# Kernel tuning notes

Measured on AMD Instinct MI355X. Metric: run time of the kernel, lower is better.

Reference implementation:

```python
import jax, jax.numpy as jnp
import numpy as np

NUM_LEVELS = 16
LEVEL_DIM = 2
BASE_RES = 32
PER_LEVEL_SCALE = 2.0
TABLE_SIZE = 2 ** 19  # padded size of every level's table
RES = np.array([int(BASE_RES * PER_LEVEL_SCALE ** i) for i in range(NUM_LEVELS)], dtype=np.float32)
SIZES = np.minimum(RES.astype(np.float64) ** 3, TABLE_SIZE).astype(np.float32)  # true table sizes
NEAR, FAR, NUM_SAMPLES = 0.1, 1.5, 64
N_RAYS = 16384


def _xavier(key, fin, fout):
    lim = float(np.sqrt(6.0 / (fin + fout)))
    return jax.random.uniform(key, (fin, fout), jnp.float32, -lim, lim)


def setup_inputs() -> dict:
    key = jax.random.key(0)
    ks = jax.random.split(key, 12)
    rays_o = jax.random.uniform(ks[0], (N_RAYS, 3), jnp.float32, -0.5, 0.5)
    d = jax.random.normal(ks[1], (N_RAYS, 3), jnp.float32)
    rays_d = d / jnp.linalg.norm(d, axis=-1, keepdims=True)
    tables = jax.random.uniform(ks[2], (NUM_LEVELS, TABLE_SIZE, LEVEL_DIM), jnp.float32, -1e-4, 1e-4)
    return {
        'rays_o': rays_o, 'rays_d': rays_d, 'tables': tables,
        'Wg0': _xavier(ks[3], 32, 64), 'bg0': jnp.zeros((64,), jnp.float32),
        'Wg1': _xavier(ks[4], 64, 64), 'bg1': jnp.zeros((64,), jnp.float32),
        'Wd': _xavier(ks[5], 64, 16), 'bd': jnp.zeros((16,), jnp.float32),
        'Wc0': _xavier(ks[6], 24, 64), 'bc0': jnp.zeros((64,), jnp.float32),
        'Wc1': _xavier(ks[7], 64, 64), 'bc1': jnp.zeros((64,), jnp.float32),
        'Wc2': _xavier(ks[8], 64, 64), 'bc2': jnp.zeros((64,), jnp.float32),
        'Wch': _xavier(ks[9], 64, 3), 'bch': jnp.zeros((3,), jnp.float32),
    }


def _hash_encode(pts, tables):
    # pts: [N, S, 3] in roughly [-1, 1]; tables: [L, T, 2]
    res = jnp.asarray(RES)            # [L]
    sizes = jnp.asarray(SIZES)        # [L]
    scaled = (pts[..., None, :] + 1.0) / 2.0 * (res[:, None] - 1.0)     # [N,S,L,3]
    scaled = jnp.clip(scaled, 0.0, res[:, None] - 1.0)
    # torch computes the flat index in float then .long() (truncation), then clamps to table size
    idx_f = scaled[..., 0] * res * res + scaled[..., 1] * res + scaled[..., 2]  # [N,S,L]
    idx = jnp.minimum(idx_f, sizes - 1.0).astype(jnp.int32)
    feats = tables[jnp.arange(NUM_LEVELS)[None, None, :], idx]          # [N,S,L,2]
    return feats.reshape(feats.shape[:-2] + (NUM_LEVELS * LEVEL_DIM,))  # [N,S,32]


def _sh_encode(d):
    # degree-4 encoder in the source only ever builds 9 features
    x, y, z = d[..., 0], d[..., 1], d[..., 2]
    return jnp.stack([jnp.full_like(x, 0.5), x, y, z,
                      x * y, x * z, y * z, x * x - y * y, 3.0 * z * z - 1.0], axis=-1)  # [N,9]


def reference(rays_o, rays_d, tables, Wg0, bg0, Wg1, bg1, Wd, bd,
              Wc0, bc0, Wc1, bc1, Wc2, bc2, Wch, bch):
    n = rays_o.shape[0]
    # --- stratified-free (eval mode) sampling along rays ---
    t = jnp.linspace(0.0, 1.0, NUM_SAMPLES, dtype=jnp.float32)
    z_vals = jnp.broadcast_to(NEAR + (FAR - NEAR) * t, (n, NUM_SAMPLES))           # [N,S]
    pts = rays_o[:, None, :] + rays_d[:, None, :] * z_vals[..., None]              # [N,S,3]
    # --- LoDAwareNeRF forward ---
    feats = _hash_encode(pts, tables)                                              # [N,S,32]
    h = jax.nn.relu(feats @ Wg0 + bg0)
    h = jax.nn.relu(h @ Wg1 + bg1)
    geo = h @ Wd + bd                                                              # [N,S,16]
    density = jax.nn.softplus(geo[..., 0] - 1.0)                                   # [N,S]
    geo_feat = geo[..., 1:]                                                        # [N,S,15]
    dir_f = jnp.broadcast_to(_sh_encode(rays_d)[:, None, :], (n, NUM_SAMPLES, 9))  # [N,S,9]
    c = jnp.concatenate([geo_feat, dir_f], axis=-1)                                # [N,S,24]
    c = jax.nn.relu(c @ Wc0 + bc0)
    c = jax.nn.relu(c @ Wc1 + bc1)
    c = jax.nn.relu(c @ Wc2 + bc2)
    color = jax.nn.sigmoid(c @ Wch + bch)                                          # [N,S,3]
    # --- volume rendering compositing ---
    dists = z_vals[..., 1:] - z_vals[..., :-1]
    dists = jnp.concatenate([dists, jnp.full_like(dists[..., :1], 1e10)], axis=-1)
    dists = dists * jnp.linalg.norm(rays_d, axis=-1, keepdims=True)
    alpha = 1.0 - jnp.exp(-density * dists)                                        # [N,S]
    T = jnp.cumprod(1.0 - alpha + 1e-10, axis=-1)
    T = jnp.concatenate([jnp.ones_like(T[..., :1]), T[..., :-1]], axis=-1)
    weights = alpha * T                                                            # [N,S]
    rgb = jnp.sum(weights[..., None] * color, axis=-2)                             # [N,3]
    depth = jnp.sum(weights * z_vals, axis=-1)                                     # [N]
    acc = jnp.sum(weights, axis=-1)                                                # [N]
    return rgb, depth, acc, weights
```

## Files before the change

### kernel.cpp

```cpp
#include <hip/hip_runtime.h>
#include <hip/hip_bf16.h>
#include <math.h>

typedef float  f32x4 __attribute__((ext_vector_type(4)));
typedef short  s16x8 __attribute__((ext_vector_type(8)));
typedef unsigned int u32x2 __attribute__((ext_vector_type(2)));
typedef unsigned int u32x4 __attribute__((ext_vector_type(4)));

constexpr int kNRays = 16384;
constexpr int kTableSize = 1 << 19;
constexpr int kOffDepth   = kNRays * 3;
constexpr int kOffAcc     = kOffDepth + kNRays;
constexpr int kOffWeights = kOffAcc + kNRays;

constexpr int kWg0 = 0;
constexpr int kWg1 = 2048;
constexpr int kWd  = 6144;
constexpr int kWc0 = 7168;
constexpr int kWc1 = 9216;
constexpr int kWc2 = 13312;
constexpr int kWch = 17408;
constexpr int kWsTotal = 18432;

__device__ __forceinline__ ushort f2bf(float x) {
    unsigned u = __float_as_uint(x);
    return (ushort)((u + 0x7FFFu + ((u >> 16) & 1u)) >> 16);
}
__device__ __forceinline__ unsigned pk2(float lo, float hi) {
    __hip_bfloat162 h = __float22bfloat162_rn(float2{lo, hi});
    return *reinterpret_cast<unsigned*>(&h);
}
__device__ __forceinline__ float sel4(float v0, float v1, float v2, float v3, int s) {
    float a = (s & 1) ? v1 : v0;
    float b = (s & 1) ? v3 : v2;
    return (s & 2) ? b : a;
}
__device__ __forceinline__ float wave_sum(float v) {
#pragma unroll
    for (int off = 32; off > 0; off >>= 1) v += __shfl_xor(v, off, 64);
    return v;
}

__global__ __launch_bounds__(256) void prep_weights(
    const float* __restrict__ Wg0, const float* __restrict__ Wg1,
    const float* __restrict__ Wd,  const float* __restrict__ Wc0,
    const float* __restrict__ Wc1, const float* __restrict__ Wc2,
    const float* __restrict__ Wch, ushort* __restrict__ ws)
{
    const int i = blockIdx.x * 256 + threadIdx.x;
    if (i >= kWsTotal) return;
    const float* W; int FIN, FOUT, KT, base; bool dperm = false;
    if (i < kWg1)      { W = Wg0; FIN = 32; FOUT = 64; KT = 1; base = kWg0; }
    else if (i < kWd)  { W = Wg1; FIN = 64; FOUT = 64; KT = 2; base = kWg1; }
    else if (i < kWc0) { W = Wd;  FIN = 64; FOUT = 16; KT = 2; base = kWd; dperm = true; }
    else if (i < kWc1) { W = Wc0; FIN = 24; FOUT = 64; KT = 1; base = kWc0; }
    else if (i < kWc2) { W = Wc1; FIN = 64; FOUT = 64; KT = 2; base = kWc1; }
    else if (i < kWch) { W = Wc2; FIN = 64; FOUT = 64; KT = 2; base = kWc2; }
    else               { W = Wch; FIN = 64; FOUT = 3;  KT = 2; base = kWch; }
    const int r = i - base;
    const int e = r & 7, l = (r >> 3) & 63, t = r >> 9;
    const int kt = t % KT, mt = t / KT;
    const int k = kt * 32 + ((l >> 4) << 3) + e;
    int j = mt * 16 + (l & 15);
    if (dperm) j = (j == 15) ? 0 : j + 1;
    float w = 0.0f;
    if (k < FIN && j < FOUT) w = W[k * FOUT + j];
    ws[i] = f2bf(w);
}

template<int KT, bool RELU>
__device__ __forceinline__ void layer64(ushort* Xw, const ushort* __restrict__ Aws,
                                        const float* __restrict__ bias,
                                        int c16, int g, int lane) {
    s16x8 B[KT][4];
#pragma unroll
    for (int kt = 0; kt < KT; ++kt)
#pragma unroll
        for (int nt = 0; nt < 4; ++nt) {
            const int col = nt * 16 + c16;
            B[kt][nt] = *(const s16x8*)&Xw[col * 64 + 8 * ((kt * 4 + g) ^ (c16 & 7))];
        }
#pragma unroll
    for (int mt = 0; mt < 4; ++mt) {
        const s16x8 A0 = *(const s16x8*)&Aws[((mt * KT + 0) * 64 + lane) * 8];
        s16x8 A1;
        if constexpr (KT == 2) A1 = *(const s16x8*)&Aws[((mt * KT + 1) * 64 + lane) * 8];
        const f32x4 b = *(const f32x4*)(bias + mt * 16 + g * 4);
        f32x4 acc[4];
#pragma unroll
        for (int nt = 0; nt < 4; ++nt) {
            acc[nt] = b;
            acc[nt] = __builtin_amdgcn_mfma_f32_16x16x32_bf16(A0, B[0][nt], acc[nt], 0, 0, 0);
            if constexpr (KT == 2)
                acc[nt] = __builtin_amdgcn_mfma_f32_16x16x32_bf16(A1, B[1][nt], acc[nt], 0, 0, 0);
        }
#pragma unroll
        for (int nt = 0; nt < 4; ++nt) {
            const int col = nt * 16 + c16;
            float x0 = acc[nt].x, x1 = acc[nt].y, x2 = acc[nt].z, x3 = acc[nt].w;
            if (RELU) {
                x0 = fmaxf(x0, 0.f); x1 = fmaxf(x1, 0.f);
                x2 = fmaxf(x2, 0.f); x3 = fmaxf(x3, 0.f);
            }
            const int a = col * 64 + 8 * ((2 * mt + (g >> 1)) ^ (c16 & 7)) + 4 * (g & 1);
            *(u32x2*)&Xw[a] = (u32x2){ pk2(x0, x1), pk2(x2, x3) };
        }
    }
}

template<int KT>
__device__ __forceinline__ void layer16(const ushort* Xw, const ushort* __restrict__ Aws,
                                        int c16, int g, int lane, f32x4 acc[4]) {
    const s16x8 A0 = *(const s16x8*)&Aws[(0 * 64 + lane) * 8];
    s16x8 A1;
    if constexpr (KT == 2) A1 = *(const s16x8*)&Aws[(1 * 64 + lane) * 8];
#pragma unroll
    for (int nt = 0; nt < 4; ++nt) {
        const int col = nt * 16 + c16;
        const s16x8 B0 = *(const s16x8*)&Xw[col * 64 + 8 * ((0 * 4 + g) ^ (c16 & 7))];
        acc[nt] = __builtin_amdgcn_mfma_f32_16x16x32_bf16(A0, B0, acc[nt], 0, 0, 0);
        if constexpr (KT == 2) {
            const s16x8 B1 = *(const s16x8*)&Xw[col * 64 + 8 * ((1 * 4 + g) ^ (c16 & 7))];
            acc[nt] = __builtin_amdgcn_mfma_f32_16x16x32_bf16(A1, B1, acc[nt], 0, 0, 0);
        }
    }
}

__global__ __launch_bounds__(256, 4) void nerf_mfma_kernel(
    const float* __restrict__ rays_o, const float* __restrict__ rays_d,
    const float* __restrict__ tables, const ushort* __restrict__ ws,
    const float* __restrict__ bg0, const float* __restrict__ bg1,
    const float* __restrict__ bd,  const float* __restrict__ bc0,
    const float* __restrict__ bc1, const float* __restrict__ bc2,
    const float* __restrict__ bch, float* __restrict__ out)
{
    __shared__ __align__(16) ushort Xs[4 * 4096];
    const int tid  = threadIdx.x;
    const int wid  = tid >> 6;
    const int lane = tid & 63;
    const int c16  = lane & 15;
    const int g    = lane >> 4;
    const int ray  = blockIdx.x * 4 + wid;
    ushort* Xw = Xs + wid * 4096;

    const float ox = rays_o[ray * 3 + 0], oy = rays_o[ray * 3 + 1], oz = rays_o[ray * 3 + 2];
    const float dx = rays_d[ray * 3 + 0], dy = rays_d[ray * 3 + 1], dz = rays_d[ray * 3 + 2];

    const float step = 1.0f / 63.0f;
    const float z  = 0.1f + 1.4f * ((float)lane * step);
    const float zn = 0.1f + 1.4f * ((float)(lane + 1) * step);

    s16x8 B0[4];
#pragma unroll
    for (int nt = 0; nt < 4; ++nt) {
        const int s = nt * 16 + c16;
        const float zs = 0.1f + 1.4f * ((float)s * step);
        const float px = ox + dx * zs, py = oy + dy * zs, pz = oz + dz * zs;
        u32x4 val;
#pragma unroll
        for (int j = 0; j < 4; ++j) {
            const int lv = g * 4 + j;
            const float res = (float)(32 << lv);
            const float rm1 = res - 1.0f;
            float sx = (px + 1.0f) * 0.5f * rm1; sx = fminf(fmaxf(sx, 0.f), rm1);
            float sy = (py + 1.0f) * 0.5f * rm1; sy = fminf(fmaxf(sy, 0.f), rm1);
            float sz = (pz + 1.0f) * 0.5f * rm1; sz = fminf(fmaxf(sz, 0.f), rm1);
            const float idxf = sx * res * res + sy * res + sz;
            const float szm1 = (lv == 0) ? 32767.f : (lv == 1) ? 262143.f : 524287.f;
            const int idx = (int)fminf(idxf, szm1);
            const float2 f2 = *reinterpret_cast<const float2*>(
                tables + ((size_t)lv * kTableSize + (size_t)idx) * 2);
            val[j] = pk2(f2.x, f2.y);
        }
        B0[nt] = *(const s16x8*)&val;
    }

#pragma unroll
    for (int mt = 0; mt < 4; ++mt) {
        const s16x8 A0 = *(const s16x8*)&ws[kWg0 + (mt * 64 + lane) * 8];
        const f32x4 b = *(const f32x4*)(bg0 + mt * 16 + g * 4);
        f32x4 acc[4];
#pragma unroll
        for (int nt = 0; nt < 4; ++nt) {
            acc[nt] = b;
            acc[nt] = __builtin_amdgcn_mfma_f32_16x16x32_bf16(A0, B0[nt], acc[nt], 0, 0, 0);
        }
#pragma unroll
        for (int nt = 0; nt < 4; ++nt) {
            const int col = nt * 16 + c16;
            const float x0 = fmaxf(acc[nt].x, 0.f), x1 = fmaxf(acc[nt].y, 0.f);
            const float x2 = fmaxf(acc[nt].z, 0.f), x3 = fmaxf(acc[nt].w, 0.f);
            const int a = col * 64 + 8 * ((2 * mt + (g >> 1)) ^ (c16 & 7)) + 4 * (g & 1);
            *(u32x2*)&Xw[a] = (u32x2){ pk2(x0, x1), pk2(x2, x3) };
        }
    }

    layer64<2, true>(Xw, ws + kWg1, bg1, c16, g, lane);

    f32x4 accd[4];
    {
        const float db0 = bd[g * 4 + 1];
        const float db1 = bd[g * 4 + 2];
        const float db2 = bd[g * 4 + 3];
        const int i3 = (g == 3) ? 0 : g * 4 + 4;
        const float db3 = bd[i3];
        const f32x4 b = { db0, db1, db2, db3 };
#pragma unroll
        for (int nt = 0; nt < 4; ++nt) accd[nt] = b;
    }
    layer16<2>(Xw, ws + kWd, c16, g, lane, accd);
    const float lgit = sel4(__shfl(accd[0].w, 48 + c16, 64),
                            __shfl(accd[1].w, 48 + c16, 64),
                            __shfl(accd[2].w, 48 + c16, 64),
                            __shfl(accd[3].w, 48 + c16, 64), g);
#pragma unroll
    for (int nt = 0; nt < 4; ++nt) {
        const int col = nt * 16 + c16;
        const int a = col * 64 + 8 * ((g >> 1) ^ (c16 & 7)) + 4 * (g & 1);
        *(u32x2*)&Xw[a] = (u32x2){ pk2(accd[nt].x, accd[nt].y), pk2(accd[nt].z, accd[nt].w) };
    }
    Xw[lane * 64 + 8 * (1 ^ (lane & 7)) + 7] = 0x3F00;
    {
        u32x4 w = { pk2(dx, dy), pk2(dz, dx * dy), pk2(dx * dz, dy * dz),
                    pk2(dx * dx - dy * dy, 3.f * dz * dz - 1.f) };
        *(u32x4*)&Xw[lane * 64 + 8 * (2 ^ (lane & 7))] = w;
    }

    layer64<1, true>(Xw, ws + kWc0, bc0, c16, g, lane);
    layer64<2, true>(Xw, ws + kWc1, bc1, c16, g, lane);
    layer64<2, true>(Xw, ws + kWc2, bc2, c16, g, lane);

    f32x4 accc[4];
    {
        const float cb0 = bch[0], cb1 = bch[1], cb2 = bch[2];
        const f32x4 b = (g == 0) ? (f32x4){ cb0, cb1, cb2, 0.f } : (f32x4){ 0.f, 0.f, 0.f, 0.f };
#pragma unroll
        for (int nt = 0; nt < 4; ++nt) accc[nt] = b;
    }
    layer16<2>(Xw, ws + kWch, c16, g, lane, accc);
    const float lr = sel4(__shfl(accc[0].x, c16, 64), __shfl(accc[1].x, c16, 64),
                          __shfl(accc[2].x, c16, 64), __shfl(accc[3].x, c16, 64), g);
    const float lgr = sel4(__shfl(accc[0].y, c16, 64), __shfl(accc[1].y, c16, 64),
                           __shfl(accc[2].y, c16, 64), __shfl(accc[3].y, c16, 64), g);
    const float lb = sel4(__shfl(accc[0].z, c16, 64), __shfl(accc[1].z, c16, 64),
                          __shfl(accc[2].z, c16, 64), __shfl(accc[3].z, c16, 64), g);

    const float cr = 1.f / (1.f + expf(-lr));
    const float cg = 1.f / (1.f + expf(-lgr));
    const float cb = 1.f / (1.f + expf(-lb));
    const float gx = lgit - 1.0f;
    const float density = fmaxf(gx, 0.f) + log1pf(expf(-fabsf(gx)));

    const float dnorm = sqrtf(dx * dx + dy * dy + dz * dz);
    float dist = (lane < 63) ? (zn - z) : 1e10f;
    dist *= dnorm;
    const float alpha = 1.0f - expf(-density * dist);
    float f = 1.0f - alpha + 1e-10f;
#pragma unroll
    for (int off = 1; off < 64; off <<= 1) {
        const float gg = __shfl_up(f, off, 64);
        if (lane >= off) f *= gg;
    }
    float T = __shfl_up(f, 1, 64);
    if (lane == 0) T = 1.0f;
    const float w = alpha * T;

    out[kOffWeights + ray * 64 + lane] = w;
    const float sr = wave_sum(w * cr);
    const float sg = wave_sum(w * cg);
    const float sb = wave_sum(w * cb);
    const float sd = wave_sum(w * z);
    const float sa = wave_sum(w);
    if (lane == 0) {
        out[ray * 3 + 0] = sr;
        out[ray * 3 + 1] = sg;
        out[ray * 3 + 2] = sb;
        out[kOffDepth + ray] = sd;
        out[kOffAcc + ray]   = sa;
    }
}

extern "C" void kernel_launch(void* const* d_in, const int* in_sizes, int n_in,
                              void* d_out, int out_size, void* d_ws, size_t ws_size,
                              hipStream_t stream) {
    const float* rays_o = (const float*)d_in[0];
    const float* rays_d = (const float*)d_in[1];
    const float* tables = (const float*)d_in[2];
    const float* Wg0 = (const float*)d_in[3];
    const float* bg0 = (const float*)d_in[4];
    const float* Wg1 = (const float*)d_in[5];
    const float* bg1 = (const float*)d_in[6];
    const float* Wd  = (const float*)d_in[7];
    const float* bd  = (const float*)d_in[8];
    const float* Wc0 = (const float*)d_in[9];
    const float* bc0 = (const float*)d_in[10];
    const float* Wc1 = (const float*)d_in[11];
    const float* bc1 = (const float*)d_in[12];
    const float* Wc2 = (const float*)d_in[13];
    const float* bc2 = (const float*)d_in[14];
    const float* Wch = (const float*)d_in[15];
    const float* bch = (const float*)d_in[16];
    float* out = (float*)d_out;
    ushort* wsp = (ushort*)d_ws;

    prep_weights<<<dim3((kWsTotal + 255) / 256), dim3(256), 0, stream>>>(
        Wg0, Wg1, Wd, Wc0, Wc1, Wc2, Wch, wsp);

    nerf_mfma_kernel<<<dim3(kNRays / 4), dim3(256), 0, stream>>>(
        rays_o, rays_d, tables, wsp,
        bg0, bg1, bd, bc0, bc1, bc2, bch, out);
}
```

Before: 80.55 us.

## Roll MLP layers into a runtime loop and pad Wc0 to two K-tiles

Replaces the four fully unrolled 64-wide hidden layers with one runtime loop (unroll 1 over layers and M tiles). Wc0 is padded to KT=2 so every layer shares the same code path, and the density head is handled inside the first iteration. The hash-encoding index math is also rewritten with fma and fmed3 clamps, using per-level base pointers. The intent is to shrink code size and register pressure at the cost of loop overhead, less cross-layer scheduling freedom, and extra zero-padded MFMAs for the Wc0 layer.

```diff
diff --git a/kernel.cpp b/kernel.cpp
--- a/kernel.cpp
+++ b/kernel.cpp
@@ -17,10 +17,10 @@
 constexpr int kWg1 = 2048;
 constexpr int kWd  = 6144;
 constexpr int kWc0 = 7168;
-constexpr int kWc1 = 9216;
-constexpr int kWc2 = 13312;
-constexpr int kWch = 17408;
-constexpr int kWsTotal = 18432;
+constexpr int kWc1 = 11264;
+constexpr int kWc2 = 15360;
+constexpr int kWch = 19456;
+constexpr int kWsTotal = 20480;
 
 __device__ __forceinline__ ushort f2bf(float x) {
     unsigned u = __float_as_uint(x);
@@ -53,7 +53,7 @@
     if (i < kWg1)      { W = Wg0; FIN = 32; FOUT = 64; KT = 1; base = kWg0; }
     else if (i < kWd)  { W = Wg1; FIN = 64; FOUT = 64; KT = 2; base = kWg1; }
     else if (i < kWc0) { W = Wd;  FIN = 64; FOUT = 16; KT = 2; base = kWd; dperm = true; }
-    else if (i < kWc1) { W = Wc0; FIN = 24; FOUT = 64; KT = 1; base = kWc0; }
+    else if (i < kWc1) { W = Wc0; FIN = 24; FOUT = 64; KT = 2; base = kWc0; }
     else if (i < kWc2) { W = Wc1; FIN = 64; FOUT = 64; KT = 2; base = kWc1; }
     else if (i < kWch) { W = Wc2; FIN = 64; FOUT = 64; KT = 2; base = kWc2; }
     else               { W = Wch; FIN = 64; FOUT = 3;  KT = 2; base = kWch; }
@@ -68,61 +68,17 @@
     ws[i] = f2bf(w);
 }
 
-template<int KT, bool RELU>
-__device__ __forceinline__ void layer64(ushort* Xw, const ushort* __restrict__ Aws,
-                                        const float* __restrict__ bias,
-                                        int c16, int g, int lane) {
-    s16x8 B[KT][4];
-#pragma unroll
-    for (int kt = 0; kt < KT; ++kt)
-#pragma unroll
-        for (int nt = 0; nt < 4; ++nt) {
-            const int col = nt * 16 + c16;
-            B[kt][nt] = *(const s16x8*)&Xw[col * 64 + 8 * ((kt * 4 + g) ^ (c16 & 7))];
-        }
-#pragma unroll
-    for (int mt = 0; mt < 4; ++mt) {
-        const s16x8 A0 = *(const s16x8*)&Aws[((mt * KT + 0) * 64 + lane) * 8];
-        s16x8 A1;
-        if constexpr (KT == 2) A1 = *(const s16x8*)&Aws[((mt * KT + 1) * 64 + lane) * 8];
-        const f32x4 b = *(const f32x4*)(bias + mt * 16 + g * 4);
-        f32x4 acc[4];
-#pragma unroll
-        for (int nt = 0; nt < 4; ++nt) {
-            acc[nt] = b;
-            acc[nt] = __builtin_amdgcn_mfma_f32_16x16x32_bf16(A0, B[0][nt], acc[nt], 0, 0, 0);
-            if constexpr (KT == 2)
-                acc[nt] = __builtin_amdgcn_mfma_f32_16x16x32_bf16(A1, B[1][nt], acc[nt], 0, 0, 0);
-        }
-#pragma unroll
-        for (int nt = 0; nt < 4; ++nt) {
-            const int col = nt * 16 + c16;
-            float x0 = acc[nt].x, x1 = acc[nt].y, x2 = acc[nt].z, x3 = acc[nt].w;
-            if (RELU) {
-                x0 = fmaxf(x0, 0.f); x1 = fmaxf(x1, 0.f);
-                x2 = fmaxf(x2, 0.f); x3 = fmaxf(x3, 0.f);
-            }
-            const int a = col * 64 + 8 * ((2 * mt + (g >> 1)) ^ (c16 & 7)) + 4 * (g & 1);
-            *(u32x2*)&Xw[a] = (u32x2){ pk2(x0, x1), pk2(x2, x3) };
-        }
-    }
-}
-
-template<int KT>
 __device__ __forceinline__ void layer16(const ushort* Xw, const ushort* __restrict__ Aws,
                                         int c16, int g, int lane, f32x4 acc[4]) {
     const s16x8 A0 = *(const s16x8*)&Aws[(0 * 64 + lane) * 8];
-    s16x8 A1;
-    if constexpr (KT == 2) A1 = *(const s16x8*)&Aws[(1 * 64 + lane) * 8];
+    const s16x8 A1 = *(const s16x8*)&Aws[(1 * 64 + lane) * 8];
 #pragma unroll
     for (int nt = 0; nt < 4; ++nt) {
         const int col = nt * 16 + c16;
         const s16x8 B0 = *(const s16x8*)&Xw[col * 64 + 8 * ((0 * 4 + g) ^ (c16 & 7))];
         acc[nt] = __builtin_amdgcn_mfma_f32_16x16x32_bf16(A0, B0, acc[nt], 0, 0, 0);
-        if constexpr (KT == 2) {
-            const s16x8 B1 = *(const s16x8*)&Xw[col * 64 + 8 * ((1 * 4 + g) ^ (c16 & 7))];
-            acc[nt] = __builtin_amdgcn_mfma_f32_16x16x32_bf16(A1, B1, acc[nt], 0, 0, 0);
-        }
+        const s16x8 B1 = *(const s16x8*)&Xw[col * 64 + 8 * ((1 * 4 + g) ^ (c16 & 7))];
+        acc[nt] = __builtin_amdgcn_mfma_f32_16x16x32_bf16(A1, B1, acc[nt], 0, 0, 0);
     }
 }
 
@@ -150,32 +106,38 @@
     const float z  = 0.1f + 1.4f * ((float)lane * step);
     const float zn = 0.1f + 1.4f * ((float)(lane + 1) * step);
 
-    s16x8 B0[4];
+    const float2* lvb[4];
+#pragma unroll
+    for (int j = 0; j < 4; ++j)
+        lvb[j] = (const float2*)tables + ((size_t)(g * 4 + j) << 19);
+
+    const float tc = (float)c16 * step;
+    s16x8 B0f[4];
 #pragma unroll
     for (int nt = 0; nt < 4; ++nt) {
-        const int s = nt * 16 + c16;
-        const float zs = 0.1f + 1.4f * ((float)s * step);
-        const float px = ox + dx * zs, py = oy + dy * zs, pz = oz + dz * zs;
+        const float ts = tc + (float)nt * (16.0f / 63.0f);
+        const float zs = fmaf(1.4f, ts, 0.1f);
+        const float px = fmaf(dx, zs, ox), py = fmaf(dy, zs, oy), pz = fmaf(dz, zs, oz);
         u32x4 val;
 #pragma unroll
         for (int j = 0; j < 4; ++j) {
             const int lv = g * 4 + j;
             const float res = (float)(32 << lv);
             const float rm1 = res - 1.0f;
-            float sx = (px + 1.0f) * 0.5f * rm1; sx = fminf(fmaxf(sx, 0.f), rm1);
-            float sy = (py + 1.0f) * 0.5f * rm1; sy = fminf(fmaxf(sy, 0.f), rm1);
-            float sz = (pz + 1.0f) * 0.5f * rm1; sz = fminf(fmaxf(sz, 0.f), rm1);
-            const float idxf = sx * res * res + sy * res + sz;
+            const float h = 0.5f * rm1;
+            const float sx = __builtin_amdgcn_fmed3f(fmaf(px, h, h), 0.f, rm1);
+            const float sy = __builtin_amdgcn_fmed3f(fmaf(py, h, h), 0.f, rm1);
+            const float sz = __builtin_amdgcn_fmed3f(fmaf(pz, h, h), 0.f, rm1);
+            const float idxf = fmaf(sx, res * res, fmaf(sy, res, sz));
             const float szm1 = (lv == 0) ? 32767.f : (lv == 1) ? 262143.f : 524287.f;
             const int idx = (int)fminf(idxf, szm1);
-            const float2 f2 = *reinterpret_cast<const float2*>(
-                tables + ((size_t)lv * kTableSize + (size_t)idx) * 2);
+            const float2 f2 = lvb[j][idx];
             val[j] = pk2(f2.x, f2.y);
         }
-        B0[nt] = *(const s16x8*)&val;
-    }
-
-#pragma unroll
+        B0f[nt] = *(const s16x8*)&val;
+    }
+
+#pragma unroll 1
     for (int mt = 0; mt < 4; ++mt) {
         const s16x8 A0 = *(const s16x8*)&ws[kWg0 + (mt * 64 + lane) * 8];
         const f32x4 b = *(const f32x4*)(bg0 + mt * 16 + g * 4);
@@ -183,7 +145,7 @@
 #pragma unroll
         for (int nt = 0; nt < 4; ++nt) {
             acc[nt] = b;
-            acc[nt] = __builtin_amdgcn_mfma_f32_16x16x32_bf16(A0, B0[nt], acc[nt], 0, 0, 0);
+            acc[nt] = __builtin_amdgcn_mfma_f32_16x16x32_bf16(A0, B0f[nt], acc[nt], 0, 0, 0);
         }
 #pragma unroll
         for (int nt = 0; nt < 4; ++nt) {
@@ -195,40 +157,72 @@
         }
     }
 
-    layer64<2, true>(Xw, ws + kWg1, bg1, c16, g, lane);
-
-    f32x4 accd[4];
-    {
-        const float db0 = bd[g * 4 + 1];
-        const float db1 = bd[g * 4 + 2];
-        const float db2 = bd[g * 4 + 3];
-        const int i3 = (g == 3) ? 0 : g * 4 + 4;
-        const float db3 = bd[i3];
-        const f32x4 b = { db0, db1, db2, db3 };
-#pragma unroll
-        for (int nt = 0; nt < 4; ++nt) accd[nt] = b;
-    }
-    layer16<2>(Xw, ws + kWd, c16, g, lane, accd);
-    const float lgit = sel4(__shfl(accd[0].w, 48 + c16, 64),
-                            __shfl(accd[1].w, 48 + c16, 64),
-                            __shfl(accd[2].w, 48 + c16, 64),
-                            __shfl(accd[3].w, 48 + c16, 64), g);
-#pragma unroll
-    for (int nt = 0; nt < 4; ++nt) {
-        const int col = nt * 16 + c16;
-        const int a = col * 64 + 8 * ((g >> 1) ^ (c16 & 7)) + 4 * (g & 1);
-        *(u32x2*)&Xw[a] = (u32x2){ pk2(accd[nt].x, accd[nt].y), pk2(accd[nt].z, accd[nt].w) };
-    }
-    Xw[lane * 64 + 8 * (1 ^ (lane & 7)) + 7] = 0x3F00;
-    {
-        u32x4 w = { pk2(dx, dy), pk2(dz, dx * dy), pk2(dx * dz, dy * dz),
-                    pk2(dx * dx - dy * dy, 3.f * dz * dz - 1.f) };
-        *(u32x4*)&Xw[lane * 64 + 8 * (2 ^ (lane & 7))] = w;
-    }
-
-    layer64<1, true>(Xw, ws + kWc0, bc0, c16, g, lane);
-    layer64<2, true>(Xw, ws + kWc1, bc1, c16, g, lane);
-    layer64<2, true>(Xw, ws + kWc2, bc2, c16, g, lane);
+    float lgit = 0.f;
+#pragma unroll 1
+    for (int li = 0; li < 4; ++li) {
+        const ushort* Aws = ws + ((li == 0) ? kWg1 : kWc0 + (li - 1) * 4096);
+        const float* bp = (li == 0) ? bg1 : (li == 1) ? bc0 : (li == 2) ? bc1 : bc2;
+        s16x8 B[2][4];
+#pragma unroll
+        for (int kt = 0; kt < 2; ++kt)
+#pragma unroll
+            for (int nt = 0; nt < 4; ++nt) {
+                const int col = nt * 16 + c16;
+                B[kt][nt] = *(const s16x8*)&Xw[col * 64 + 8 * ((kt * 4 + g) ^ (c16 & 7))];
+            }
+#pragma unroll 1
+        for (int mt = 0; mt < 4; ++mt) {
+            const s16x8 A0 = *(const s16x8*)&Aws[((mt * 2 + 0) * 64 + lane) * 8];
+            const s16x8 A1 = *(const s16x8*)&Aws[((mt * 2 + 1) * 64 + lane) * 8];
+            const f32x4 b = *(const f32x4*)(bp + mt * 16 + g * 4);
+            f32x4 acc[4];
+#pragma unroll
+            for (int nt = 0; nt < 4; ++nt) {
+                acc[nt] = b;
+                acc[nt] = __builtin_amdgcn_mfma_f32_16x16x32_bf16(A0, B[0][nt], acc[nt], 0, 0, 0);
+                acc[nt] = __builtin_amdgcn_mfma_f32_16x16x32_bf16(A1, B[1][nt], acc[nt], 0, 0, 0);
+            }
+#pragma unroll
+            for (int nt = 0; nt < 4; ++nt) {
+                const int col = nt * 16 + c16;
+                const float x0 = fmaxf(acc[nt].x, 0.f), x1 = fmaxf(acc[nt].y, 0.f);
+                const float x2 = fmaxf(acc[nt].z, 0.f), x3 = fmaxf(acc[nt].w, 0.f);
+                const int a = col * 64 + 8 * ((2 * mt + (g >> 1)) ^ (c16 & 7)) + 4 * (g & 1);
+                *(u32x2*)&Xw[a] = (u32x2){ pk2(x0, x1), pk2(x2, x3) };
+            }
+        }
+        if (li == 0) {
+            f32x4 accd[4];
+            {
+                const float db0 = bd[g * 4 + 1];
+                const float db1 = bd[g * 4 + 2];
+                const float db2 = bd[g * 4 + 3];
+                const int i3 = (g == 3) ? 0 : g * 4 + 4;
+                const float db3 = bd[i3];
+                const f32x4 b = { db0, db1, db2, db3 };
+#pragma unroll
+                for (int nt = 0; nt < 4; ++nt) accd[nt] = b;
+            }
+            layer16(Xw, ws + kWd, c16, g, lane, accd);
+            lgit = sel4(__shfl(accd[0].w, 48 + c16, 64),
+                        __shfl(accd[1].w, 48 + c16, 64),
+                        __shfl(accd[2].w, 48 + c16, 64),
+                        __shfl(accd[3].w, 48 + c16, 64), g);
+#pragma unroll
+            for (int nt = 0; nt < 4; ++nt) {
+                const int col = nt * 16 + c16;
+                const int a = col * 64 + 8 * ((g >> 1) ^ (c16 & 7)) + 4 * (g & 1);
+                *(u32x2*)&Xw[a] = (u32x2){ pk2(accd[nt].x, accd[nt].y),
+                                           pk2(accd[nt].z, accd[nt].w) };
+            }
+            Xw[lane * 64 + 8 * (1 ^ (lane & 7)) + 7] = 0x3F00;
+            {
+                u32x4 w = { pk2(dx, dy), pk2(dz, dx * dy), pk2(dx * dz, dy * dz),
+                            pk2(dx * dx - dy * dy, 3.f * dz * dz - 1.f) };
+                *(u32x4*)&Xw[lane * 64 + 8 * (2 ^ (lane & 7))] = w;
+            }
+        }
+    }
 
     f32x4 accc[4];
     {
@@ -237,7 +231,7 @@
 #pragma unroll
         for (int nt = 0; nt < 4; ++nt) accc[nt] = b;
     }
-    layer16<2>(Xw, ws + kWch, c16, g, lane, accc);
+    layer16(Xw, ws + kWch, c16, g, lane, accc);
     const float lr = sel4(__shfl(accc[0].x, c16, 64), __shfl(accc[1].x, c16, 64),
                           __shfl(accc[2].x, c16, 64), __shfl(accc[3].x, c16, 64), g);
     const float lgr = sel4(__shfl(accc[0].y, c16, 64), __shfl(accc[1].y, c16, 64),
```

New measurement: 85.69 us. 6.4% more time.
